# Optimization experiments

Measured on AMD Instinct MI355X. Metric: run time of the kernel, lower is better.

The kernel has to match this reference:

```python
import jax, jax.numpy as jnp
import numpy as np

COS_EPS = 1e-8      # torch.nn.CosineSimilarity default eps
VAL_EPS = 1e-18     # denominator eps for relative value distance
MEAN_EPS = 1e-13    # masked_mean tiny value (allennlp-style)


def setup_inputs() -> dict:
    key = jax.random.key(0)
    k1, k2, k3 = jax.random.split(key, 3)
    bs, nsl, hs = 32, 1024, 768
    embeds = jax.random.normal(k1, (bs, nsl, hs), dtype=jnp.float32)
    ground_truth = jax.random.randint(k2, (bs, nsl), 0, 10000, dtype=jnp.int32)
    number_mask = jax.random.randint(k3, (bs, nsl), 0, 2, dtype=jnp.int32).astype(jnp.bool_)
    return {"embeds": embeds, "ground_truth": ground_truth, "number_mask": number_mask}


def reference(embeds, ground_truth, number_mask):
    bs, nsl, hs = embeds.shape
    # Pairwise cosine similarity via normalized GEMM (no bs*nsl*nsl*hs expansion).
    # torch CosineSimilarity: dot / (max(||x||,eps) * max(||y||,eps))
    norms = jnp.maximum(jnp.linalg.norm(embeds, axis=-1, keepdims=True), COS_EPS)
    xn = embeds / norms                                   # [bs, nsl, hs]
    cos = jnp.einsum('bih,bjh->bij', xn, xn)              # [bs, nsl, nsl]
    embeds_cosine = 1.0 - cos

    # Pair mask: outer product of number_mask, strictly upper triangular.
    pair_mask = number_mask[:, :, None] & number_mask[:, None, :]
    tri = jnp.triu(jnp.ones((nsl, nsl), dtype=jnp.bool_), k=1)
    pair_mask = (pair_mask & tri).astype(jnp.float32)     # [bs, nsl, nsl]

    # Relative value distance: 2|x-y| / (|x|+|y|+eps)
    gt = ground_truth.astype(jnp.float32)
    x = gt[:, None, :]                                    # x[b,i,j] = gt[b,j]
    y = gt[:, :, None]                                    # y[b,i,j] = gt[b,i]
    val_dist = 2.0 * jnp.abs(x - y) / (jnp.abs(x) + jnp.abs(y) + VAL_EPS)

    sq = jnp.square(embeds_cosine - val_dist)             # [bs, nsl, nsl]
    num = jnp.sum(sq * pair_mask, axis=(1, 2))            # masked sum per sample
    den = jnp.sum(pair_mask, axis=(1, 2)) + MEAN_EPS
    loss = jnp.sqrt(num / den).mean()
    return loss
```

## Files before the change

kernel.cpp:

```cpp
#include <hip/hip_runtime.h>
#include <math.h>

#define BSZ 32
#define NSL 1024
#define HS  768
#define BM  128
#define BK  32
#define NKS (HS / BK)
#define NTILE (NSL / BM)
#define TILES_PER_BATCH 36
#define NWG (BSZ * TILES_PER_BATCH)

typedef __attribute__((ext_vector_type(8))) unsigned short u16x8;
typedef __attribute__((ext_vector_type(4))) float f32x4;

__device__ __forceinline__ unsigned short f2bf(float x) {
  unsigned u = __float_as_uint(x);
  unsigned r = (u + 0x7FFFu + ((u >> 16) & 1u)) >> 16;
  return (unsigned short)r;
}

__device__ __forceinline__ void gload_lds16(const void* g, void* l) {
  __builtin_amdgcn_global_load_lds((__attribute__((address_space(1))) void*)(void*)g,
                                   (__attribute__((address_space(3))) void*)l, 16, 0, 0);
}

__global__ void detect_kernel(const unsigned int* __restrict__ mraw, int* __restrict__ flag) {
  __shared__ int okInt, okF32;
  if (threadIdx.x == 0) { okInt = 1; okF32 = 1; }
  __syncthreads();
  int badI = 0, badF = 0;
  for (int i = threadIdx.x; i < 8192; i += 256) {
    unsigned v = mraw[i];
    if (v != 0u && v != 1u) badI = 1;
    if (v != 0u && v != 0x3F800000u) badF = 1;
  }
  if (badI) atomicAnd(&okInt, 0);
  if (badF) atomicAnd(&okF32, 0);
  __syncthreads();
  if (threadIdx.x == 0) *flag = okInt ? 0 : (okF32 ? 1 : 2);
}

__global__ __launch_bounds__(256) void convert_kernel(const void* __restrict__ mraw,
                                                      const int* __restrict__ gt,
                                                      const int* __restrict__ flag,
                                                      float* __restrict__ gtf,
                                                      float* __restrict__ maskf,
                                                      float* __restrict__ cnt) {
  int i = blockIdx.x * 256 + threadIdx.x;
  int f = *flag;
  bool m;
  if (f == 0)      m = ((const int*)mraw)[i] != 0;
  else if (f == 1) m = ((const float*)mraw)[i] != 0.0f;
  else             m = ((const unsigned char*)mraw)[i] != 0;
  float mf = m ? 1.0f : 0.0f;
  maskf[i] = mf;
  gtf[i] = (float)gt[i];
  float c = mf;
  #pragma unroll
  for (int off = 32; off; off >>= 1) c += __shfl_down(c, off);
  if ((threadIdx.x & 63) == 0) atomicAdd(&cnt[i >> 10], c);
}

__global__ __launch_bounds__(256) void norm_kernel(const float* __restrict__ embeds,
                                                   unsigned short* __restrict__ xn,
                                                   float* __restrict__ invn,
                                                   int writeXn) {
  int w = threadIdx.x >> 6, lane = threadIdx.x & 63;
  int row = blockIdx.x * 4 + w;
  const float* src = embeds + (size_t)row * HS;
  float4 v[3];
  float ss = 0.0f;
  #pragma unroll
  for (int q = 0; q < 3; ++q) {
    v[q] = *(const float4*)(src + q * 256 + lane * 4);
    ss += v[q].x * v[q].x + v[q].y * v[q].y + v[q].z * v[q].z + v[q].w * v[q].w;
  }
  #pragma unroll
  for (int off = 32; off; off >>= 1) ss += __shfl_xor(ss, off);
  float inv = 1.0f / fmaxf(sqrtf(ss), 1e-8f);
  if (writeXn) {
    unsigned short* dst = xn + (size_t)row * HS;
    #pragma unroll
    for (int q = 0; q < 3; ++q) {
      ushort4 h;
      h.x = f2bf(v[q].x * inv); h.y = f2bf(v[q].y * inv);
      h.z = f2bf(v[q].z * inv); h.w = f2bf(v[q].w * inv);
      *(ushort4*)(dst + q * 256 + lane * 4) = h;
    }
  } else if (lane == 0) {
    invn[row] = inv;
  }
}

template<int STAGE_F32>
__global__ __launch_bounds__(256) void gram_kernel(const float* __restrict__ embeds,
                                                   const unsigned short* __restrict__ xn,
                                                   const float* __restrict__ invn,
                                                   const float* __restrict__ gtf,
                                                   const float* __restrict__ maskf,
                                                   float* __restrict__ num) {
  __shared__ __align__(16) unsigned short lA[BM * BK];
  __shared__ __align__(16) unsigned short lB[BM * BK];
  __shared__ float gtR[BM], gtC[BM], mR[BM], mC[BM], ivR[BM], ivC[BM];
  __shared__ float red[4];

  int blk = blockIdx.x;
  int swz = (blk & 7) * (NWG / 8) + (blk >> 3);
  int b = swz / TILES_PER_BATCH;
  int t = swz % TILES_PER_BATCH;
  int ti = 0;
  { int c = NTILE; while (t >= c) { t -= c; --c; ++ti; } }
  int tj = ti + t;

  const int tid = threadIdx.x;
  const int w = tid >> 6;
  const int lane = tid & 63;
  const int wr = w >> 1, wc = w & 1;
  const int Ra = ti * BM, Rb = tj * BM;

  if (tid < BM) {
    int ia = b * NSL + Ra + tid;
    int ib = b * NSL + Rb + tid;
    gtR[tid] = gtf[ia]; mR[tid] = maskf[ia];
    gtC[tid] = gtf[ib]; mC[tid] = maskf[ib];
    if constexpr (STAGE_F32 != 0) { ivR[tid] = invn[ia]; ivC[tid] = invn[ib]; }
  }
  __syncthreads();

  f32x4 acc[4][4];
  #pragma unroll
  for (int m = 0; m < 4; ++m)
    #pragma unroll
    for (int n = 0; n < 4; ++n)
      #pragma unroll
      for (int r = 0; r < 4; ++r) acc[m][n][r] = 0.0f;

  for (int ks = 0; ks < NKS; ++ks) {
    const int kbase = ks * BK;
    if constexpr (STAGE_F32 == 0) {
      #pragma unroll
      for (int q = 0; q < 2; ++q) {
        int L = q * 256 + tid;
        int row = L >> 2, pos = L & 3;
        int c = pos ^ ((row >> 1) & 3);
        const unsigned short* gaA = xn + (size_t)(b * NSL + Ra + row) * HS + kbase + c * 8;
        const unsigned short* gaB = xn + (size_t)(b * NSL + Rb + row) * HS + kbase + c * 8;
        unsigned short* ldA = &lA[(q * 256 + w * 64) * 8];
        unsigned short* ldB = &lB[(q * 256 + w * 64) * 8];
        gload_lds16(gaA, ldA);
        gload_lds16(gaB, ldB);
      }
    } else {
      #pragma unroll
      for (int q = 0; q < 2; ++q) {
        int L = q * 256 + tid;
        int row = L >> 2, pos = L & 3;
        int c = pos ^ ((row >> 1) & 3);
        const float* gaA = embeds + (size_t)(b * NSL + Ra + row) * HS + kbase + c * 8;
        const float* gaB = embeds + (size_t)(b * NSL + Rb + row) * HS + kbase + c * 8;
        float4 a0 = *(const float4*)gaA;
        float4 a1 = *(const float4*)(gaA + 4);
        float4 b0 = *(const float4*)gaB;
        float4 b1 = *(const float4*)(gaB + 4);
        float sa = ivR[row], sb = ivC[row];
        u16x8 ha, hb;
        ha[0] = f2bf(a0.x * sa); ha[1] = f2bf(a0.y * sa);
        ha[2] = f2bf(a0.z * sa); ha[3] = f2bf(a0.w * sa);
        ha[4] = f2bf(a1.x * sa); ha[5] = f2bf(a1.y * sa);
        ha[6] = f2bf(a1.z * sa); ha[7] = f2bf(a1.w * sa);
        hb[0] = f2bf(b0.x * sb); hb[1] = f2bf(b0.y * sb);
        hb[2] = f2bf(b0.z * sb); hb[3] = f2bf(b0.w * sb);
        hb[4] = f2bf(b1.x * sb); hb[5] = f2bf(b1.y * sb);
        hb[6] = f2bf(b1.z * sb); hb[7] = f2bf(b1.w * sb);
        *(u16x8*)&lA[row * BK + pos * 8] = ha;
        *(u16x8*)&lB[row * BK + pos * 8] = hb;
      }
    }
    __syncthreads();

    u16x8 af[4], bfv[4];
    const int kc = lane >> 4;
    #pragma unroll
    for (int m = 0; m < 4; ++m) {
      int row = wr * 64 + m * 16 + (lane & 15);
      af[m] = *(const u16x8*)&lA[row * BK + ((kc ^ ((row >> 1) & 3)) * 8)];
    }
    #pragma unroll
    for (int n = 0; n < 4; ++n) {
      int row = wc * 64 + n * 16 + (lane & 15);
      bfv[n] = *(const u16x8*)&lB[row * BK + ((kc ^ ((row >> 1) & 3)) * 8)];
    }
    #pragma unroll
    for (int m = 0; m < 4; ++m)
      #pragma unroll
      for (int n = 0; n < 4; ++n)
        asm volatile("v_mfma_f32_16x16x32_bf16 %0, %1, %2, %0"
                     : "+v"(acc[m][n]) : "v"(af[m]), "v"(bfv[n]));
    __syncthreads();
  }

  asm volatile("s_nop 7\n\ts_nop 7");

  float lsum = 0.0f;
  const bool diag = (ti == tj);
  #pragma unroll
  for (int m = 0; m < 4; ++m) {
    #pragma unroll
    for (int n = 0; n < 4; ++n) {
      int ljl = wc * 64 + n * 16 + (lane & 15);
      float gj = gtC[ljl], mj = mC[ljl];
      #pragma unroll
      for (int r = 0; r < 4; ++r) {
        int lil = wr * 64 + m * 16 + (lane >> 4) * 4 + r;
        float gi = gtR[lil], mi_ = mR[lil];
        float cosd = 1.0f - acc[m][n][r];
        float vd = 2.0f * fabsf(gi - gj) / (fabsf(gi) + fabsf(gj) + 1e-18f);
        float d = cosd - vd;
        float pm = mi_ * mj;
        if (diag) pm = (lil < ljl) ? pm : 0.0f;
        lsum += d * d * pm;
      }
    }
  }
  #pragma unroll
  for (int off = 32; off; off >>= 1) lsum += __shfl_down(lsum, off);
  if (lane == 0) red[w] = lsum;
  __syncthreads();
  if (tid == 0) atomicAdd(&num[b], red[0] + red[1] + red[2] + red[3]);
}

__global__ void final_kernel(const float* __restrict__ num, const float* __restrict__ cnt,
                             float* __restrict__ out) {
  int l = threadIdx.x;
  float v = 0.0f;
  if (l < BSZ) {
    float c = cnt[l];
    float den = 0.5f * c * (c - 1.0f) + 1e-13f;
    v = sqrtf(num[l] / den);
  }
  #pragma unroll
  for (int off = 32; off; off >>= 1) v += __shfl_down(v, off);
  if (l == 0) out[0] = v * (1.0f / 32.0f);
}

extern "C" void kernel_launch(void* const* d_in, const int* in_sizes, int n_in,
                              void* d_out, int out_size, void* d_ws, size_t ws_size,
                              hipStream_t stream) {
  const float* embeds = (const float*)d_in[0];
  const int* gt = (const int*)d_in[1];
  const void* mask = d_in[2];
  float* out = (float*)d_out;

  char* ws = (char*)d_ws;
  float* num   = (float*)(ws + 0);
  float* cnt   = (float*)(ws + 128);
  int*   flag  = (int*)(ws + 256);
  float* gtf   = (float*)(ws + 512);
  float* maskf = (float*)(ws + 512 + 131072);
  float* invn  = (float*)(ws + 512 + 262144);
  unsigned short* xn = (unsigned short*)(ws + 512 + 393216);
  const size_t need_xn = 512 + 393216 + (size_t)BSZ * NSL * HS * 2;

  hipMemsetAsync(d_ws, 0, 512, stream);
  detect_kernel<<<1, 256, 0, stream>>>((const unsigned int*)mask, flag);
  convert_kernel<<<BSZ * NSL / 256, 256, 0, stream>>>(mask, gt, flag, gtf, maskf, cnt);

  int useXn = (ws_size >= need_xn) ? 1 : 0;
  norm_kernel<<<BSZ * NSL / 4, 256, 0, stream>>>(embeds, xn, invn, useXn);
  if (useXn)
    gram_kernel<0><<<NWG, 256, 0, stream>>>(embeds, xn, invn, gtf, maskf, num);
  else
    gram_kernel<1><<<NWG, 256, 0, stream>>>(embeds, xn, invn, gtf, maskf, num);
  final_kernel<<<1, 64, 0, stream>>>(num, cnt, out);
}
```

Baseline: 223.6 us.

## Double-buffer LDS in gram kernel and fold convert/final kernels into it

Double-buffers the A/B LDS tiles so the next k-slice is staged while MFMAs run on the current one, leaving one barrier per k-step instead of two. Removes the convert kernel: the gram kernel reads ground truth and mask directly, and diagonal tiles accumulate the per-batch mask counts. Removes the final kernel with a last-block-done counter that computes the loss inside the gram kernel. This cuts launches and global traffic, at the cost of twice the LDS and a grid-wide atomic at the end.

```diff
diff --git a/kernel.cpp b/kernel.cpp
--- a/kernel.cpp
+++ b/kernel.cpp
@@ -41,25 +41,12 @@
   if (threadIdx.x == 0) *flag = okInt ? 0 : (okF32 ? 1 : 2);
 }
 
-__global__ __launch_bounds__(256) void convert_kernel(const void* __restrict__ mraw,
-                                                      const int* __restrict__ gt,
-                                                      const int* __restrict__ flag,
-                                                      float* __restrict__ gtf,
-                                                      float* __restrict__ maskf,
-                                                      float* __restrict__ cnt) {
-  int i = blockIdx.x * 256 + threadIdx.x;
-  int f = *flag;
+__device__ __forceinline__ float mask_at(const void* mraw, int f, int idx) {
   bool m;
-  if (f == 0)      m = ((const int*)mraw)[i] != 0;
-  else if (f == 1) m = ((const float*)mraw)[i] != 0.0f;
-  else             m = ((const unsigned char*)mraw)[i] != 0;
-  float mf = m ? 1.0f : 0.0f;
-  maskf[i] = mf;
-  gtf[i] = (float)gt[i];
-  float c = mf;
-  #pragma unroll
-  for (int off = 32; off; off >>= 1) c += __shfl_down(c, off);
-  if ((threadIdx.x & 63) == 0) atomicAdd(&cnt[i >> 10], c);
+  if (f == 0)      m = ((const int*)mraw)[idx] != 0;
+  else if (f == 1) m = ((const float*)mraw)[idx] != 0.0f;
+  else             m = ((const unsigned char*)mraw)[idx] != 0;
+  return m ? 1.0f : 0.0f;
 }
 
 __global__ __launch_bounds__(256) void norm_kernel(const float* __restrict__ embeds,
@@ -97,13 +84,18 @@
 __global__ __launch_bounds__(256) void gram_kernel(const float* __restrict__ embeds,
                                                    const unsigned short* __restrict__ xn,
                                                    const float* __restrict__ invn,
-                                                   const float* __restrict__ gtf,
-                                                   const float* __restrict__ maskf,
-                                                   float* __restrict__ num) {
-  __shared__ __align__(16) unsigned short lA[BM * BK];
-  __shared__ __align__(16) unsigned short lB[BM * BK];
+                                                   const int* __restrict__ gt,
+                                                   const void* __restrict__ mraw,
+                                                   const int* __restrict__ flag,
+                                                   float* __restrict__ num,
+                                                   float* __restrict__ cnt,
+                                                   int* __restrict__ done,
+                                                   float* __restrict__ out) {
+  __shared__ __align__(16) unsigned short lA[2][BM * BK];
+  __shared__ __align__(16) unsigned short lB[2][BM * BK];
   __shared__ float gtR[BM], gtC[BM], mR[BM], mC[BM], ivR[BM], ivC[BM];
   __shared__ float red[4];
+  __shared__ int lastFlag;
 
   int blk = blockIdx.x;
   int swz = (blk & 7) * (NWG / 8) + (blk >> 3);
@@ -120,13 +112,13 @@
   const int Ra = ti * BM, Rb = tj * BM;
 
   if (tid < BM) {
+    int f = *flag;
     int ia = b * NSL + Ra + tid;
     int ib = b * NSL + Rb + tid;
-    gtR[tid] = gtf[ia]; mR[tid] = maskf[ia];
-    gtC[tid] = gtf[ib]; mC[tid] = maskf[ib];
+    gtR[tid] = (float)gt[ia]; mR[tid] = mask_at(mraw, f, ia);
+    gtC[tid] = (float)gt[ib]; mC[tid] = mask_at(mraw, f, ib);
     if constexpr (STAGE_F32 != 0) { ivR[tid] = invn[ia]; ivC[tid] = invn[ib]; }
   }
-  __syncthreads();
 
   f32x4 acc[4][4];
   #pragma unroll
@@ -136,27 +128,21 @@
       #pragma unroll
       for (int r = 0; r < 4; ++r) acc[m][n][r] = 0.0f;
 
-  for (int ks = 0; ks < NKS; ++ks) {
+  auto stage = [&](int buf, int ks) {
     const int kbase = ks * BK;
-    if constexpr (STAGE_F32 == 0) {
-      #pragma unroll
-      for (int q = 0; q < 2; ++q) {
-        int L = q * 256 + tid;
-        int row = L >> 2, pos = L & 3;
-        int c = pos ^ ((row >> 1) & 3);
+    #pragma unroll
+    for (int q = 0; q < 2; ++q) {
+      int L = q * 256 + tid;
+      int row = L >> 2, pos = L & 3;
+      int c = pos ^ ((row >> 1) & 3);
+      if constexpr (STAGE_F32 == 0) {
         const unsigned short* gaA = xn + (size_t)(b * NSL + Ra + row) * HS + kbase + c * 8;
         const unsigned short* gaB = xn + (size_t)(b * NSL + Rb + row) * HS + kbase + c * 8;
-        unsigned short* ldA = &lA[(q * 256 + w * 64) * 8];
-        unsigned short* ldB = &lB[(q * 256 + w * 64) * 8];
+        unsigned short* ldA = &lA[buf][(q * 256 + w * 64) * 8];
+        unsigned short* ldB = &lB[buf][(q * 256 + w * 64) * 8];
         gload_lds16(gaA, ldA);
         gload_lds16(gaB, ldB);
-      }
-    } else {
-      #pragma unroll
-      for (int q = 0; q < 2; ++q) {
-        int L = q * 256 + tid;
-        int row = L >> 2, pos = L & 3;
-        int c = pos ^ ((row >> 1) & 3);
+      } else {
         const float* gaA = embeds + (size_t)(b * NSL + Ra + row) * HS + kbase + c * 8;
         const float* gaB = embeds + (size_t)(b * NSL + Rb + row) * HS + kbase + c * 8;
         float4 a0 = *(const float4*)gaA;
@@ -173,23 +159,31 @@
         hb[2] = f2bf(b0.z * sb); hb[3] = f2bf(b0.w * sb);
         hb[4] = f2bf(b1.x * sb); hb[5] = f2bf(b1.y * sb);
         hb[6] = f2bf(b1.z * sb); hb[7] = f2bf(b1.w * sb);
-        *(u16x8*)&lA[row * BK + pos * 8] = ha;
-        *(u16x8*)&lB[row * BK + pos * 8] = hb;
+        *(u16x8*)&lA[buf][row * BK + pos * 8] = ha;
+        *(u16x8*)&lB[buf][row * BK + pos * 8] = hb;
       }
     }
-    __syncthreads();
+  };
+
+  if constexpr (STAGE_F32 != 0) __syncthreads();
+  stage(0, 0);
+  __syncthreads();
+
+  int cur = 0;
+  for (int ks = 0; ks < NKS; ++ks) {
+    if (ks + 1 < NKS) stage(cur ^ 1, ks + 1);
 
     u16x8 af[4], bfv[4];
     const int kc = lane >> 4;
     #pragma unroll
     for (int m = 0; m < 4; ++m) {
       int row = wr * 64 + m * 16 + (lane & 15);
-      af[m] = *(const u16x8*)&lA[row * BK + ((kc ^ ((row >> 1) & 3)) * 8)];
+      af[m] = *(const u16x8*)&lA[cur][row * BK + ((kc ^ ((row >> 1) & 3)) * 8)];
     }
     #pragma unroll
     for (int n = 0; n < 4; ++n) {
       int row = wc * 64 + n * 16 + (lane & 15);
-      bfv[n] = *(const u16x8*)&lB[row * BK + ((kc ^ ((row >> 1) & 3)) * 8)];
+      bfv[n] = *(const u16x8*)&lB[cur][row * BK + ((kc ^ ((row >> 1) & 3)) * 8)];
     }
     #pragma unroll
     for (int m = 0; m < 4; ++m)
@@ -198,6 +192,7 @@
         asm volatile("v_mfma_f32_16x16x32_bf16 %0, %1, %2, %0"
                      : "+v"(acc[m][n]) : "v"(af[m]), "v"(bfv[n]));
     __syncthreads();
+    cur ^= 1;
   }
 
   asm volatile("s_nop 7\n\ts_nop 7");
@@ -228,20 +223,35 @@
   if (lane == 0) red[w] = lsum;
   __syncthreads();
   if (tid == 0) atomicAdd(&num[b], red[0] + red[1] + red[2] + red[3]);
-}
-
-__global__ void final_kernel(const float* __restrict__ num, const float* __restrict__ cnt,
-                             float* __restrict__ out) {
-  int l = threadIdx.x;
-  float v = 0.0f;
-  if (l < BSZ) {
-    float c = cnt[l];
-    float den = 0.5f * c * (c - 1.0f) + 1e-13f;
-    v = sqrtf(num[l] / den);
-  }
-  #pragma unroll
-  for (int off = 32; off; off >>= 1) v += __shfl_down(v, off);
-  if (l == 0) out[0] = v * (1.0f / 32.0f);
+
+  if (diag) {
+    __syncthreads();
+    float pc = (tid < BM) ? mR[tid] : 0.0f;
+    #pragma unroll
+    for (int off = 32; off; off >>= 1) pc += __shfl_down(pc, off);
+    if (lane == 0) red[w] = pc;
+    __syncthreads();
+    if (tid == 0) atomicAdd(&cnt[b], red[0] + red[1] + red[2] + red[3]);
+  }
+
+  __threadfence();
+  if (tid == 0) {
+    int old = atomicAdd(done, 1);
+    lastFlag = (old == NWG - 1);
+  }
+  __syncthreads();
+  if (lastFlag && w == 0) {
+    float v = 0.0f;
+    if (lane < BSZ) {
+      float n = atomicAdd(&num[lane], 0.0f);
+      float c = atomicAdd(&cnt[lane], 0.0f);
+      float den = 0.5f * c * (c - 1.0f) + 1e-13f;
+      v = sqrtf(n / den);
+    }
+    #pragma unroll
+    for (int off = 32; off; off >>= 1) v += __shfl_down(v, off);
+    if (lane == 0) out[0] = v * (1.0f / 32.0f);
+  }
 }
 
 extern "C" void kernel_launch(void* const* d_in, const int* in_sizes, int n_in,
@@ -256,21 +266,18 @@
   float* num   = (float*)(ws + 0);
   float* cnt   = (float*)(ws + 128);
   int*   flag  = (int*)(ws + 256);
-  float* gtf   = (float*)(ws + 512);
-  float* maskf = (float*)(ws + 512 + 131072);
-  float* invn  = (float*)(ws + 512 + 262144);
-  unsigned short* xn = (unsigned short*)(ws + 512 + 393216);
-  const size_t need_xn = 512 + 393216 + (size_t)BSZ * NSL * HS * 2;
+  int*   done  = (int*)(ws + 260);
+  float* invn  = (float*)(ws + 512);
+  unsigned short* xn = (unsigned short*)(ws + 512 + 131072);
+  const size_t need_xn = 512 + 131072 + (size_t)BSZ * NSL * HS * 2;
 
   hipMemsetAsync(d_ws, 0, 512, stream);
   detect_kernel<<<1, 256, 0, stream>>>((const unsigned int*)mask, flag);
-  convert_kernel<<<BSZ * NSL / 256, 256, 0, stream>>>(mask, gt, flag, gtf, maskf, cnt);
 
   int useXn = (ws_size >= need_xn) ? 1 : 0;
   norm_kernel<<<BSZ * NSL / 4, 256, 0, stream>>>(embeds, xn, invn, useXn);
   if (useXn)
-    gram_kernel<0><<<NWG, 256, 0, stream>>>(embeds, xn, invn, gtf, maskf, num);
+    gram_kernel<0><<<NWG, 256, 0, stream>>>(embeds, xn, invn, gt, mask, flag, num, cnt, done, out);
   else
-    gram_kernel<1><<<NWG, 256, 0, stream>>>(embeds, xn, invn, gtf, maskf, num);
-  final_kernel<<<1, 64, 0, stream>>>(num, cnt, out);
-}
+    gram_kernel<1><<<NWG, 256, 0, stream>>>(embeds, xn, invn, gt, mask, flag, num, cnt, done, out);
+}
```

Result: slower. 293.7 us (+31.3%).
